# Kernel tuning notes

Hardware: AMD Instinct MI355X
Metric: run time of the kernel (lower is better)

The kernel has to match this reference:

```python
import jax, jax.numpy as jnp
import numpy as np

N, E, B = 50000, 400000, 50
F_IN, HID, HEADS, F_OUT = 128, 32, 8, 64
HC = HID * HEADS  # 256


def gat_conv(x, src, dst, W, a_s, a_d, b, n):
    """PyG-style GATConv (concat=True, negative_slope=0.2), inference mode."""
    H, C = a_s.shape
    h = (x @ W).reshape(n, H, C)                       # [N,H,C]
    alpha_s = (h * a_s).sum(-1)                        # [N,H]
    alpha_d = (h * a_d).sum(-1)                        # [N,H]
    logits = jax.nn.leaky_relu(alpha_s[src] + alpha_d[dst], 0.2)  # [E,H]
    m = jax.ops.segment_max(logits, dst, num_segments=n)
    m = jnp.where(jnp.isfinite(m), m, 0.0)
    e = jnp.exp(logits - m[dst])
    den = jax.ops.segment_sum(e, dst, num_segments=n)
    alpha = e / (den[dst] + 1e-16)                     # segment softmax over dst
    out = jax.ops.segment_sum(h[src] * alpha[:, :, None], dst, num_segments=n)
    return out.reshape(n, H * C) + b


def setup_inputs() -> dict:
    key = jax.random.key(0)
    ks = jax.random.split(key, 24)
    s = 0.1
    inp = {
        "x": jax.random.normal(ks[0], (N, F_IN), jnp.float32),
        "edge_index": jax.random.randint(ks[1], (2, E), 0, N),
        "batch": jnp.sort(jax.random.randint(ks[2], (N,), 0, B)),
        "W1": jax.random.normal(ks[3], (F_IN, HC), jnp.float32) * s,
        "a_src1": jax.random.normal(ks[4], (HEADS, HID), jnp.float32) * s,
        "a_dst1": jax.random.normal(ks[5], (HEADS, HID), jnp.float32) * s,
        "b1": jnp.zeros((HC,), jnp.float32),
        "W2": jax.random.normal(ks[6], (HC, HC), jnp.float32) * s,
        "a_src2": jax.random.normal(ks[7], (1, HC), jnp.float32) * s,
        "a_dst2": jax.random.normal(ks[8], (1, HC), jnp.float32) * s,
        "b2": jnp.zeros((HC,), jnp.float32),
        "W3": jax.random.normal(ks[9], (HC, HC), jnp.float32) * s,
        "a_src3": jax.random.normal(ks[10], (1, HC), jnp.float32) * s,
        "a_dst3": jax.random.normal(ks[11], (1, HC), jnp.float32) * s,
        "b3": jnp.zeros((HC,), jnp.float32),
        "W4": jax.random.normal(ks[12], (HC, F_OUT), jnp.float32) * s,
        "a_src4": jax.random.normal(ks[13], (1, F_OUT), jnp.float32) * s,
        "a_dst4": jax.random.normal(ks[14], (1, F_OUT), jnp.float32) * s,
        "b4": jnp.zeros((F_OUT,), jnp.float32),
        "Wl": jax.random.normal(ks[15], (F_OUT, 1), jnp.float32) * s,
        "bl": jnp.zeros((1,), jnp.float32),
    }
    return inp


def reference(x, edge_index, batch, W1, a_src1, a_dst1, b1, W2, a_src2, a_dst2, b2,
              W3, a_src3, a_dst3, b3, W4, a_src4, a_dst4, b4, Wl, bl):
    n = x.shape[0]
    loop = jnp.arange(n)
    src = jnp.concatenate([edge_index[0], loop])  # add self loops (PyG default)
    dst = jnp.concatenate([edge_index[1], loop])
    x = jax.nn.elu(gat_conv(x, src, dst, W1, a_src1, a_dst1, b1, n))
    x = jax.nn.elu(gat_conv(x, src, dst, W2, a_src2, a_dst2, b2, n))
    x = jax.nn.elu(gat_conv(x, src, dst, W3, a_src3, a_dst3, b3, n))
    x_gat = gat_conv(x, src, dst, W4, a_src4, a_dst4, b4, n)
    # to_dense_batch(x_gat, batch).mean(dim=1): sum per graph / max graph size
    counts = jax.ops.segment_sum(jnp.ones((n,), x_gat.dtype), batch, num_segments=B)
    max_nodes = counts.max()
    pooled = jax.ops.segment_sum(x_gat, batch, num_segments=B) / max_nodes  # [B,F_OUT]
    return pooled @ Wl + bl  # [B,1]
```

## Files before the change

### kernel.cpp

```cpp
#include <hip/hip_runtime.h>
#include <math.h>


typedef __attribute__((ext_vector_type(8))) short short8;
typedef __attribute__((ext_vector_type(4))) float f32x4;

__device__ __forceinline__ unsigned short f2bf(float f) {
  unsigned int u = __builtin_bit_cast(unsigned int, f);
  unsigned int r = u + 0x7FFFu + ((u >> 16) & 1u);
  return (unsigned short)(r >> 16);
}
__device__ __forceinline__ float bf2f(unsigned short h) {
  unsigned int u = ((unsigned int)h) << 16;
  return __builtin_bit_cast(float, u);
}
__device__ __forceinline__ unsigned short f2h(float f) {
  _Float16 h = (_Float16)f;
  return __builtin_bit_cast(unsigned short, h);
}
__device__ __forceinline__ float h2f(unsigned short u) {
  return (float)__builtin_bit_cast(_Float16, u);
}

__device__ __forceinline__ void fma_mix_lo(float& acc, unsigned int packed, float w) {
  asm("v_fma_mix_f32 %0, %1, %2, %0 op_sel_hi:[1,0,0]"
      : "+v"(acc) : "v"(packed), "v"(w));
}
__device__ __forceinline__ void fma_mix_hi(float& acc, unsigned int packed, float w) {
  asm("v_fma_mix_f32 %0, %1, %2, %0 op_sel:[1,0,0] op_sel_hi:[1,0,0]"
      : "+v"(acc) : "v"(packed), "v"(w));
}

__device__ __forceinline__ void gload16(const unsigned short* g, unsigned short* l) {
  __builtin_amdgcn_global_load_lds(
      (const __attribute__((address_space(1))) void*)g,
      (__attribute__((address_space(3))) void*)l, 16, 0, 0);
}

template<int H>
__global__ __launch_bounds__(256) void k_gemm_mfma(
    const unsigned short* __restrict__ A2, const unsigned short* __restrict__ Wt,
    unsigned short* __restrict__ C, const float* __restrict__ avec_s,
    const float* __restrict__ avec_d, float* __restrict__ outS,
    float* __restrict__ outD, int M, int Kb, int Nc)
{
  __shared__ unsigned short lds[12288];
  unsigned short* As = lds;
  unsigned short* Bs = lds + 4096;
  const int tid = threadIdx.x;
  const int w = tid >> 6, l = tid & 63;
  const int row0 = blockIdx.x * 64, col0 = blockIdx.y * 128;
  const int wr = w >> 1, wc = w & 1;
  const int fr = l & 15, kg = l >> 4;
  const int xr = (fr & 7) << 4;
  const int sK = Kb;
  const int csrc = 8 * ((l & 7) ^ ((l >> 3) & 7));
  const int lrow = l >> 3;

  f32x4 acc[2][4];
  #pragma unroll
  for (int i = 0; i < 2; i++)
    #pragma unroll
    for (int j = 0; j < 4; j++) acc[i][j] = (f32x4){0.f, 0.f, 0.f, 0.f};

  for (int kp = 0; kp < sK; kp += 64) {
    #pragma unroll
    for (int i = 0; i < 2; i++) {
      int q = w * 2 + i;
      gload16(&A2[(size_t)(row0 + q * 8 + lrow) * sK + (kp + csrc)], &As[q * 512]);
    }
    #pragma unroll
    for (int i = 0; i < 4; i++) {
      int q = w * 4 + i;
      gload16(&Wt[(size_t)(col0 + q * 8 + lrow) * sK + (kp + csrc)], &Bs[q * 512]);
    }
    __syncthreads();
    #pragma unroll
    for (int kk = 0; kk < 2; kk++) {
      short8 a[2], b[4];
      #pragma unroll
      for (int mi = 0; mi < 2; mi++) {
        int r = wr * 32 + mi * 16 + fr;
        int off = r * 128 + ((kk * 64 + kg * 16) ^ xr);
        a[mi] = *(const short8*)((const char*)As + off);
      }
      #pragma unroll
      for (int ni = 0; ni < 4; ni++) {
        int c = wc * 64 + ni * 16 + fr;
        int off = c * 128 + ((kk * 64 + kg * 16) ^ xr);
        b[ni] = *(const short8*)((const char*)Bs + off);
      }
      #pragma unroll
      for (int mi = 0; mi < 2; mi++)
        #pragma unroll
        for (int ni = 0; ni < 4; ni++)
          acc[mi][ni] = __builtin_amdgcn_mfma_f32_16x16x32_bf16(
              a[mi], b[ni], acc[mi][ni], 0, 0, 0);
    }
    __syncthreads();
  }

  #pragma unroll
  for (int mi = 0; mi < 2; mi++)
    #pragma unroll
    for (int ni = 0; ni < 4; ni++)
      #pragma unroll
      for (int rr = 0; rr < 4; rr++) {
        int row = wr * 32 + mi * 16 + kg * 4 + rr;
        int c = wc * 64 + ni * 16 + fr;
        int sc = c ^ (((row >> 1) & 7) << 3);
        lds[row * 128 + sc] = f2h(acc[mi][ni][rr]);
      }
  __syncthreads();

  constexpr int RW = (H == 8) ? 4 : 16;
  const int Ch = Nc / H;
  const int rbase = tid >> 4;
  const int cc = tid & 15;
  const int c0 = cc * 8;
  const int gc0 = col0 + c0;
  float as8[8], ad8[8];
  #pragma unroll
  for (int j = 0; j < 8; j++) {
    bool ok = (gc0 + j) < Nc;
    as8[j] = ok ? avec_s[gc0 + j] : 0.f;
    ad8[j] = ok ? avec_d[gc0 + j] : 0.f;
  }
  #pragma unroll
  for (int i = 0; i < 4; i++) {
    int row = rbase + i * 16;
    int gr = row0 + row;
    int scc = c0 ^ (((row >> 1) & 7) << 3);
    short8 cv = *(const short8*)&lds[row * 128 + scc];
    if (gr < M && gc0 < Nc)
      *(short8*)&C[(size_t)gr * Nc + gc0] = cv;
    float ps = 0.f, pd = 0.f;
    #pragma unroll
    for (int j = 0; j < 8; j++) {
      float cf = h2f((unsigned short)cv[j]);
      ps = fmaf(cf, as8[j], ps);
      pd = fmaf(cf, ad8[j], pd);
    }
    #pragma unroll
    for (int off = 1; off < RW; off <<= 1) {
      ps += __shfl_xor(ps, off);
      pd += __shfl_xor(pd, off);
    }
    if ((tid & (RW - 1)) == 0 && gr < M) {
      int head = gc0 / Ch;
      atomicAdd(&outS[gr * H + head], ps);
      atomicAdd(&outD[gr * H + head], pd);
    }
  }
}

__global__ __launch_bounds__(256) void k_packX(const float* __restrict__ x,
    unsigned short* __restrict__ A2, int N, int Mpad)
{
  int row = blockIdx.x * 8 + (threadIdx.x >> 5);
  int c = (threadIdx.x & 31) * 4;
  if (row >= Mpad) return;
  float4 v = make_float4(0.f, 0.f, 0.f, 0.f);
  if (row < N) v = *(const float4*)&x[(size_t)row * 128 + c];
  unsigned short h0 = f2bf(v.x), h1 = f2bf(v.y), h2 = f2bf(v.z), h3 = f2bf(v.w);
  *(uint2*)&A2[(size_t)row * 128 + c] =
      make_uint2((unsigned)h0 | ((unsigned)h1 << 16),
                 (unsigned)h2 | ((unsigned)h3 << 16));
}

__device__ __forceinline__ void packW_one(const float* __restrict__ W,
    unsigned short* __restrict__ Wt, int K, int NC, int idx)
{
  int c = idx / K, k = idx % K;
  unsigned short o = 0;
  if (c < NC) o = f2bf(W[(size_t)k * NC + c]);
  Wt[(size_t)c * K + k] = o;
}

__global__ void k_packW_all(const float* __restrict__ W1, const float* __restrict__ W2,
    const float* __restrict__ W3, const float* __restrict__ W4,
    unsigned short* __restrict__ t1, unsigned short* __restrict__ t2,
    unsigned short* __restrict__ t3, unsigned short* __restrict__ t4)
{
  int idx = blockIdx.x * 256 + threadIdx.x;
  if (idx < 32768)            packW_one(W1, t1, 128, 256, idx);
  else if (idx < 98304)       packW_one(W2, t2, 256, 256, idx - 32768);
  else if (idx < 163840)      packW_one(W3, t3, 256, 256, idx - 98304);
  else if (idx < 196608)      packW_one(W4, t4, 256,  64, idx - 163840);
}

template<int H>
__global__ void k_wcomp(const float* __restrict__ aS, const float* __restrict__ aD,
    const int* __restrict__ col, const int* __restrict__ rid,
    float* __restrict__ wbuf, int M)
{
  int idx = blockIdx.x * 256 + threadIdx.x;
  if (idx >= M) return;
  int e = idx / H, hd = idx % H;
  int s = col[e], r = rid[e];
  float lg = aS[s * H + hd] + aD[r * H + hd];
  lg = fmaxf(lg, 0.2f * lg);
  wbuf[idx] = __expf(lg);
}

template<int H, int HC, int ELU, int SPLIT>
__global__ __launch_bounds__(256) void k_aggregate(const unsigned short* __restrict__ h,
    const float* __restrict__ wbuf,
    const int* __restrict__ rowptr, const int* __restrict__ col,
    const float* __restrict__ bias, float* __restrict__ xout,
    unsigned short* __restrict__ a2out, int N)
{
  constexpr int VEC = HC / 64;
  constexpr int C = HC / H;
  constexpr int CH = (H == 8) ? 8 : 64;
  __shared__ float wlds[4][64];
  int wave = threadIdx.x >> 6, lane = threadIdx.x & 63;
  int row = blockIdx.x * 4 + wave;
  if (row >= N) return;
  const int cb = lane * VEC;
  const int hdg = cb / C;
  int s0 = rowptr[row], s1 = rowptr[row + 1];

  float den = 0.f;
  float acc[VEC];
  #pragma unroll
  for (int v = 0; v < VEC; v++) acc[v] = 0.f;

  for (int base = s0; base < s1; base += CH) {
    int cnt = min(CH, s1 - base);
    int eo = (H == 8) ? (lane >> 3) : lane;
    bool valid = eo < cnt;
    int s = col[valid ? (base + eo) : (s1 - 1)];
    float wv = valid ? wbuf[(unsigned)(base * H) + lane] : 0.f;
    float d = wv;
    if constexpr (H == 8) {
      d += __shfl_xor(d, 8); d += __shfl_xor(d, 16); d += __shfl_xor(d, 32);
      wlds[wave][lane] = wv;
    } else {
      #pragma unroll
      for (int off = 1; off < 64; off <<= 1) d += __shfl_xor(d, off);
    }
    den += d;
    if (H == 8) {
      asm volatile("s_waitcnt lgkmcnt(0)" ::: "memory");
    }
    #pragma unroll 4
    for (int j = 0; j < cnt; j++) {
      int sj = __builtin_amdgcn_readlane(s, (H == 8) ? (j * 8) : j);
      float wj;
      if constexpr (H == 8) {
        wj = wlds[wave][j * 8 + hdg];
      } else {
        wj = __builtin_bit_cast(float,
              __builtin_amdgcn_readlane(__builtin_bit_cast(int, wv), j));
      }
      unsigned off = (unsigned)sj * HC + cb;
      if constexpr (VEC == 4) {
        uint2 raw = *(const uint2*)(h + off);
        fma_mix_lo(acc[0], raw.x, wj);
        fma_mix_hi(acc[1], raw.x, wj);
        fma_mix_lo(acc[2], raw.y, wj);
        fma_mix_hi(acc[3], raw.y, wj);
      } else {
        unsigned int raw = h[off];
        fma_mix_lo(acc[0], raw, wj);
      }
    }
  }
  if (H == 8) den = __shfl(den, hdg);
  float inv = 1.f / (den + 1e-16f);
  float o[VEC];
  #pragma unroll
  for (int v = 0; v < VEC; v++) {
    float t = acc[v] * inv + bias[cb + v];
    if (ELU) t = t > 0.f ? t : expm1f(t);
    o[v] = t;
  }
  if constexpr (SPLIT) {
    unsigned short hi[4];
    #pragma unroll
    for (int v = 0; v < 4; v++) hi[v] = f2bf(o[v]);
    *(uint2*)&a2out[(size_t)row * HC + cb] =
        make_uint2((unsigned)hi[0] | ((unsigned)hi[1] << 16),
                   (unsigned)hi[2] | ((unsigned)hi[3] << 16));
  } else if constexpr (VEC == 4) {
    *(float4*)&xout[(size_t)row * HC + cb] = make_float4(o[0], o[1], o[2], o[3]);
  } else {
    xout[(size_t)row * HC + cb] = o[0];
  }
}

__global__ void k_init(int* deg, float* pool, unsigned short* A2, int N, int B,
                       int Mpad) {
  int i = blockIdx.x * 256 + threadIdx.x;
  if (i < N) deg[i] = 1;
  if (i < B * 64) pool[i] = 0.f;
  int padn = (Mpad - N) * 256;
  if (i < padn) A2[(size_t)N * 256 + i] = 0;
}

__global__ void k_deg(const int* __restrict__ ei, int* deg, int E) {
  int e = blockIdx.x * 256 + threadIdx.x;
  if (e < E) atomicAdd(&deg[ei[E + e]], 1);
}

__global__ __launch_bounds__(256) void k_scan1(const int* __restrict__ deg,
                                               int* csum, int N, int chunk) {
  int bid = blockIdx.x, t = threadIdx.x;
  int lo = bid * chunk, hi = min(lo + chunk, N);
  int s = 0;
  for (int i = lo + t; i < hi; i += 256) s += deg[i];
  #pragma unroll
  for (int off = 32; off; off >>= 1) s += __shfl_xor(s, off);
  __shared__ int sh[4];
  if ((t & 63) == 0) sh[t >> 6] = s;
  __syncthreads();
  if (t == 0) csum[bid] = sh[0] + sh[1] + sh[2] + sh[3];
}

__global__ __launch_bounds__(256) void k_scan2(const int* __restrict__ csum,
    int* coff, const int* __restrict__ bat, int* cnt, int N, int B) {
  __shared__ int s[256];
  int t = threadIdx.x;
  int v0 = csum[t];
  s[t] = v0;
  for (int off = 1; off < 256; off <<= 1) {
    __syncthreads();
    int v = (t >= off) ? s[t - off] : 0;
    __syncthreads();
    s[t] += v;
  }
  __syncthreads();
  coff[t] = s[t] - v0;
  if (t < B) {
    int lo0 = 0, hi0 = N;
    while (lo0 < hi0) { int mid = (lo0 + hi0) >> 1; if (bat[mid] < t) lo0 = mid + 1; else hi0 = mid; }
    int lo1 = lo0, hi1 = N;
    while (lo1 < hi1) { int mid = (lo1 + hi1) >> 1; if (bat[mid] < t + 1) lo1 = mid + 1; else hi1 = mid; }
    cnt[t] = lo1 - lo0;
  }
}

__global__ __launch_bounds__(256) void k_scan3(const int* __restrict__ deg,
    const int* __restrict__ coff, int* rowptr, int* cursor, int N, int chunk) {
  __shared__ int s[256];
  int bid = blockIdx.x, t = threadIdx.x;
  int i = bid * chunk + t;
  int v = (t < chunk && i < N) ? deg[i] : 0;
  s[t] = v;
  for (int off = 1; off < 256; off <<= 1) {
    __syncthreads();
    int x = (t >= off) ? s[t - off] : 0;
    __syncthreads();
    s[t] += x;
  }
  __syncthreads();
  int excl = s[t] - v + coff[bid];
  if (t < chunk && i < N) {
    rowptr[i] = excl;
    cursor[i] = excl;
    if (i == N - 1) rowptr[N] = excl + v;
  }
}

__global__ void k_scatter(const int* __restrict__ ei, int* cursor, int* col,
                          int* rid, int E, int N) {
  int idx = blockIdx.x * 256 + threadIdx.x;
  if (idx >= E + N) return;
  int s, d;
  if (idx < E) { s = ei[idx]; d = ei[E + idx]; }
  else         { s = d = idx - E; }
  int pos = atomicAdd(&cursor[d], 1);
  col[pos] = s;
  rid[pos] = d;
}

__global__ __launch_bounds__(256) void k_pool(const float* __restrict__ xg,
    const int* __restrict__ bat, float* pool, int N) {
  int lane = threadIdx.x & 63, w = threadIdx.x >> 6;
  int base = (blockIdx.x * 4 + w) * 16;
  if (base >= N) return;
  int end = min(base + 16, N);
  float local = 0.f;
  int curb = bat[base];
  for (int n = base; n < end; n++) {
    int b = bat[n];
    if (b != curb) {
      atomicAdd(&pool[curb * 64 + lane], local);
      local = 0.f; curb = b;
    }
    local += xg[(size_t)n * 64 + lane];
  }
  atomicAdd(&pool[curb * 64 + lane], local);
}

__global__ void k_final(const float* __restrict__ pool, const int* __restrict__ cnt,
    const float* __restrict__ Wl, const float* __restrict__ bl,
    float* __restrict__ out, int B) {
  int lane = threadIdx.x;
  int c = (lane < B) ? cnt[lane] : 0;
  #pragma unroll
  for (int off = 32; off; off >>= 1) c = max(c, __shfl_xor(c, off));
  float invm = 1.f / (float)c;
  float wl = Wl[lane];
  for (int b = 0; b < B; b++) {
    float ps = pool[b * 64 + lane] * wl;
    #pragma unroll
    for (int off = 32; off; off >>= 1) ps += __shfl_xor(ps, off);
    if (lane == 0) out[b] = ps * invm + bl[0];
  }
}

extern "C" void kernel_launch(void* const* d_in, const int* in_sizes, int n_in,
                              void* d_out, int out_size, void* d_ws, size_t ws_size,
                              hipStream_t stream)
{
  (void)n_in; (void)ws_size;
  const float* x   = (const float*)d_in[0];
  const int*   ei  = (const int*)d_in[1];
  const int*   bat = (const int*)d_in[2];
  const float* W1  = (const float*)d_in[3];
  const float* as1 = (const float*)d_in[4];
  const float* ad1 = (const float*)d_in[5];
  const float* b1  = (const float*)d_in[6];
  const float* W2  = (const float*)d_in[7];
  const float* as2 = (const float*)d_in[8];
  const float* ad2 = (const float*)d_in[9];
  const float* b2  = (const float*)d_in[10];
  const float* W3  = (const float*)d_in[11];
  const float* as3 = (const float*)d_in[12];
  const float* ad3 = (const float*)d_in[13];
  const float* b3  = (const float*)d_in[14];
  const float* W4  = (const float*)d_in[15];
  const float* as4 = (const float*)d_in[16];
  const float* ad4 = (const float*)d_in[17];
  const float* b4  = (const float*)d_in[18];
  const float* Wl  = (const float*)d_in[19];
  const float* bl  = (const float*)d_in[20];
  float* out = (float*)d_out;

  const int N = in_sizes[0] / 128;
  const int E = in_sizes[1] / 2;
  const int B = out_size;
  const int Mpad = ((N + 127) / 128) * 128;
  const int EN = E + N;

  char* p = (char*)d_ws;
  auto alloc = [&](size_t bytes) -> void* {
    void* r = (void*)p;
    p += ((bytes + 255) & ~(size_t)255);
    return r;
  };
  unsigned short* A2 = (unsigned short*)alloc((size_t)Mpad * 256 * 2);
  unsigned short* hbuf = (unsigned short*)alloc((size_t)N * 256 * 2);
  unsigned short* w2t1 = (unsigned short*)alloc((size_t)256 * 128 * 2);
  unsigned short* w2t2 = (unsigned short*)alloc((size_t)256 * 256 * 2);
  unsigned short* w2t3 = (unsigned short*)alloc((size_t)256 * 256 * 2);
  unsigned short* w2t4 = (unsigned short*)alloc((size_t)128 * 256 * 2);
  float* aAll  = (float*)alloc((size_t)N * 22 * 4);
  float* aSb   = aAll;
  float* aDb   = aAll + (size_t)N * 11;
  float* wbuf  = (float*)alloc((size_t)EN * 8 * 4);
  int*   deg   = (int*)alloc((size_t)N * 4);
  int*   rowptr= (int*)alloc((size_t)(N + 1) * 4);
  int*   cursor= (int*)alloc((size_t)N * 4);
  int*   col   = (int*)alloc((size_t)EN * 4);
  int*   rid   = (int*)alloc((size_t)EN * 4);
  int*   csum  = (int*)alloc(256 * 4);
  int*   coff  = (int*)alloc(256 * 4);
  float* pool  = (float*)alloc((size_t)B * 64 * 4);
  int*   cnt   = (int*)alloc((size_t)B * 4);
  float* xpool = (float*)A2;

  const int chunk = (N + 255) / 256;
  dim3 T(256);

  k_init<<<dim3((N + 255) / 256), T, 0, stream>>>(deg, pool, A2, N, B, Mpad);
  k_deg<<<dim3((E + 255) / 256), T, 0, stream>>>(ei, deg, E);
  k_scan1<<<dim3(256), T, 0, stream>>>(deg, csum, N, chunk);
  k_scan2<<<dim3(1), T, 0, stream>>>(csum, coff, bat, cnt, N, B);
  k_scan3<<<dim3(256), T, 0, stream>>>(deg, coff, rowptr, cursor, N, chunk);
  k_scatter<<<dim3((EN + 255) / 256), T, 0, stream>>>(ei, cursor, col, rid, E, N);
  hipMemsetAsync(aAll, 0, (size_t)N * 22 * 4, stream);

  k_packX<<<dim3(Mpad / 8), T, 0, stream>>>(x, A2, N, Mpad);
  k_packW_all<<<dim3(768), T, 0, stream>>>(W1, W2, W3, W4, w2t1, w2t2, w2t3, w2t4);

  dim3 nwav((N + 3) / 4);
  dim3 g2(Mpad / 64, 2), g1(Mpad / 64, 1);
  dim3 gw8((EN * 8 + 255) / 256), gw1((EN + 255) / 256);

  float* aS1 = aSb;                 float* aD1 = aDb;
  float* aS2 = aSb + (size_t)N * 8; float* aD2 = aDb + (size_t)N * 8;
  float* aS3 = aSb + (size_t)N * 9; float* aD3 = aDb + (size_t)N * 9;
  float* aS4 = aSb + (size_t)N * 10;float* aD4 = aDb + (size_t)N * 10;

  k_gemm_mfma<8><<<g2, T, 0, stream>>>(A2, w2t1, hbuf, as1, ad1, aS1, aD1, N, 128, 256);
  k_wcomp<8><<<gw8, T, 0, stream>>>(aS1, aD1, col, rid, wbuf, EN * 8);
  k_aggregate<8, 256, 1, 1><<<nwav, T, 0, stream>>>(hbuf, wbuf, rowptr, col, b1,
                                                    nullptr, A2, N);
  k_gemm_mfma<1><<<g2, T, 0, stream>>>(A2, w2t2, hbuf, as2, ad2, aS2, aD2, N, 256, 256);
  k_wcomp<1><<<gw1, T, 0, stream>>>(aS2, aD2, col, rid, wbuf, EN);
  k_aggregate<1, 256, 1, 1><<<nwav, T, 0, stream>>>(hbuf, wbuf, rowptr, col, b2,
                                                    nullptr, A2, N);
  k_gemm_mfma<1><<<g2, T, 0, stream>>>(A2, w2t3, hbuf, as3, ad3, aS3, aD3, N, 256, 256);
  k_wcomp<1><<<gw1, T, 0, stream>>>(aS3, aD3, col, rid, wbuf, EN);
  k_aggregate<1, 256, 1, 1><<<nwav, T, 0, stream>>>(hbuf, wbuf, rowptr, col, b3,
                                                    nullptr, A2, N);
  k_gemm_mfma<1><<<g1, T, 0, stream>>>(A2, w2t4, hbuf, as4, ad4, aS4, aD4, N, 256, 64);
  k_wcomp<1><<<gw1, T, 0, stream>>>(aS4, aD4, col, rid, wbuf, EN);
  k_aggregate<1, 64, 0, 0><<<nwav, T, 0, stream>>>(hbuf, wbuf, rowptr, col, b4,
                                                   xpool, nullptr, N);

  k_pool<<<dim3((N + 63) / 64), T, 0, stream>>>(xpool, bat, pool, N);
  k_final<<<dim3(1), dim3(64), 0, stream>>>(pool, cnt, Wl, bl, out, B);
}
```

Before: 419.2 us.

## Use one-wave blocks for aggregation and split HC=64 layer across edge groups

Aggregation kernels now launch one 64-thread block per destination row instead of four rows per 256-thread block, which reduces tail imbalance from rows with uneven degree. The final 64-channel layer is restructured so that four 16-lane groups each process a different edge in parallel, using 4-wide loads, with a cross-group shuffle reduction at the end. Before, that layer used one scalar load per lane. The x packing kernel is also merged into the weight packing kernel to save one launch. The risk is more blocks to schedule and more LDS round trips.

```diff
diff --git a/kernel.cpp b/kernel.cpp
--- a/kernel.cpp
+++ b/kernel.cpp
@@ -154,20 +154,6 @@
   }
 }
 
-__global__ __launch_bounds__(256) void k_packX(const float* __restrict__ x,
-    unsigned short* __restrict__ A2, int N, int Mpad)
-{
-  int row = blockIdx.x * 8 + (threadIdx.x >> 5);
-  int c = (threadIdx.x & 31) * 4;
-  if (row >= Mpad) return;
-  float4 v = make_float4(0.f, 0.f, 0.f, 0.f);
-  if (row < N) v = *(const float4*)&x[(size_t)row * 128 + c];
-  unsigned short h0 = f2bf(v.x), h1 = f2bf(v.y), h2 = f2bf(v.z), h3 = f2bf(v.w);
-  *(uint2*)&A2[(size_t)row * 128 + c] =
-      make_uint2((unsigned)h0 | ((unsigned)h1 << 16),
-                 (unsigned)h2 | ((unsigned)h3 << 16));
-}
-
 __device__ __forceinline__ void packW_one(const float* __restrict__ W,
     unsigned short* __restrict__ Wt, int K, int NC, int idx)
 {
@@ -177,16 +163,30 @@
   Wt[(size_t)c * K + k] = o;
 }
 
-__global__ void k_packW_all(const float* __restrict__ W1, const float* __restrict__ W2,
+__global__ void k_pack_all(const float* __restrict__ W1, const float* __restrict__ W2,
     const float* __restrict__ W3, const float* __restrict__ W4,
     unsigned short* __restrict__ t1, unsigned short* __restrict__ t2,
-    unsigned short* __restrict__ t3, unsigned short* __restrict__ t4)
+    unsigned short* __restrict__ t3, unsigned short* __restrict__ t4,
+    const float* __restrict__ x, unsigned short* __restrict__ A2,
+    int N, int Mpad)
 {
   int idx = blockIdx.x * 256 + threadIdx.x;
   if (idx < 32768)            packW_one(W1, t1, 128, 256, idx);
   else if (idx < 98304)       packW_one(W2, t2, 256, 256, idx - 32768);
   else if (idx < 163840)      packW_one(W3, t3, 256, 256, idx - 98304);
   else if (idx < 196608)      packW_one(W4, t4, 256,  64, idx - 163840);
+  else {
+    int t = idx - 196608;
+    int row = t >> 5;
+    if (row >= Mpad) return;
+    int c = (t & 31) * 4;
+    float4 v = make_float4(0.f, 0.f, 0.f, 0.f);
+    if (row < N) v = *(const float4*)&x[(size_t)row * 128 + c];
+    unsigned short h0 = f2bf(v.x), h1 = f2bf(v.y), h2 = f2bf(v.z), h3 = f2bf(v.w);
+    *(uint2*)&A2[(size_t)row * 128 + c] =
+        make_uint2((unsigned)h0 | ((unsigned)h1 << 16),
+                   (unsigned)h2 | ((unsigned)h3 << 16));
+  }
 }
 
 template<int H>
@@ -204,89 +204,128 @@
 }
 
 template<int H, int HC, int ELU, int SPLIT>
-__global__ __launch_bounds__(256) void k_aggregate(const unsigned short* __restrict__ h,
+__global__ __launch_bounds__(64) void k_aggregate(const unsigned short* __restrict__ h,
     const float* __restrict__ wbuf,
     const int* __restrict__ rowptr, const int* __restrict__ col,
     const float* __restrict__ bias, float* __restrict__ xout,
     unsigned short* __restrict__ a2out, int N)
 {
-  constexpr int VEC = HC / 64;
-  constexpr int C = HC / H;
-  constexpr int CH = (H == 8) ? 8 : 64;
-  __shared__ float wlds[4][64];
-  int wave = threadIdx.x >> 6, lane = threadIdx.x & 63;
-  int row = blockIdx.x * 4 + wave;
+  const int lane = threadIdx.x;
+  const int row = blockIdx.x;
   if (row >= N) return;
-  const int cb = lane * VEC;
-  const int hdg = cb / C;
   int s0 = rowptr[row], s1 = rowptr[row + 1];
-
   float den = 0.f;
-  float acc[VEC];
-  #pragma unroll
-  for (int v = 0; v < VEC; v++) acc[v] = 0.f;
-
-  for (int base = s0; base < s1; base += CH) {
-    int cnt = min(CH, s1 - base);
-    int eo = (H == 8) ? (lane >> 3) : lane;
-    bool valid = eo < cnt;
-    int s = col[valid ? (base + eo) : (s1 - 1)];
-    float wv = valid ? wbuf[(unsigned)(base * H) + lane] : 0.f;
-    float d = wv;
-    if constexpr (H == 8) {
-      d += __shfl_xor(d, 8); d += __shfl_xor(d, 16); d += __shfl_xor(d, 32);
-      wlds[wave][lane] = wv;
-    } else {
-      #pragma unroll
-      for (int off = 1; off < 64; off <<= 1) d += __shfl_xor(d, off);
-    }
-    den += d;
-    if (H == 8) {
-      asm volatile("s_waitcnt lgkmcnt(0)" ::: "memory");
-    }
-    #pragma unroll 4
-    for (int j = 0; j < cnt; j++) {
-      int sj = __builtin_amdgcn_readlane(s, (H == 8) ? (j * 8) : j);
-      float wj;
+
+  if constexpr (HC == 256) {
+    constexpr int C = HC / H;
+    constexpr int CH = (H == 8) ? 8 : 64;
+    __shared__ float wlds[(H == 8) ? 64 : 1];
+    const int cb = lane * 4;
+    const int hdg = cb / C;
+    float acc[4] = {0.f, 0.f, 0.f, 0.f};
+    for (int base = s0; base < s1; base += CH) {
+      int cnt = min(CH, s1 - base);
+      int eo = (H == 8) ? (lane >> 3) : lane;
+      bool valid = eo < cnt;
+      int s = col[valid ? (base + eo) : (s1 - 1)];
+      float wv = valid ? wbuf[(unsigned)(base * H) + lane] : 0.f;
+      float d = wv;
       if constexpr (H == 8) {
-        wj = wlds[wave][j * 8 + hdg];
+        d += __shfl_xor(d, 8); d += __shfl_xor(d, 16); d += __shfl_xor(d, 32);
+        wlds[lane] = wv;
       } else {
-        wj = __builtin_bit_cast(float,
-              __builtin_amdgcn_readlane(__builtin_bit_cast(int, wv), j));
-      }
-      unsigned off = (unsigned)sj * HC + cb;
-      if constexpr (VEC == 4) {
+        #pragma unroll
+        for (int off = 1; off < 64; off <<= 1) d += __shfl_xor(d, off);
+      }
+      den += d;
+      if (H == 8) {
+        asm volatile("s_waitcnt lgkmcnt(0)" ::: "memory");
+      }
+      #pragma unroll 4
+      for (int j = 0; j < cnt; j++) {
+        int sj = __builtin_amdgcn_readlane(s, (H == 8) ? (j * 8) : j);
+        float wj;
+        if constexpr (H == 8) {
+          wj = wlds[j * 8 + hdg];
+        } else {
+          wj = __builtin_bit_cast(float,
+                __builtin_amdgcn_readlane(__builtin_bit_cast(int, wv), j));
+        }
+        unsigned off = (unsigned)sj * HC + cb;
         uint2 raw = *(const uint2*)(h + off);
         fma_mix_lo(acc[0], raw.x, wj);
         fma_mix_hi(acc[1], raw.x, wj);
         fma_mix_lo(acc[2], raw.y, wj);
         fma_mix_hi(acc[3], raw.y, wj);
-      } else {
-        unsigned int raw = h[off];
-        fma_mix_lo(acc[0], raw, wj);
-      }
-    }
-  }
-  if (H == 8) den = __shfl(den, hdg);
-  float inv = 1.f / (den + 1e-16f);
-  float o[VEC];
-  #pragma unroll
-  for (int v = 0; v < VEC; v++) {
-    float t = acc[v] * inv + bias[cb + v];
-    if (ELU) t = t > 0.f ? t : expm1f(t);
-    o[v] = t;
-  }
-  if constexpr (SPLIT) {
-    unsigned short hi[4];
-    #pragma unroll
-    for (int v = 0; v < 4; v++) hi[v] = f2bf(o[v]);
-    *(uint2*)&a2out[(size_t)row * HC + cb] =
-        make_uint2((unsigned)hi[0] | ((unsigned)hi[1] << 16),
-                   (unsigned)hi[2] | ((unsigned)hi[3] << 16));
-  } else if constexpr (VEC == 4) {
-    *(float4*)&xout[(size_t)row * HC + cb] = make_float4(o[0], o[1], o[2], o[3]);
+      }
+    }
+    if (H == 8) den = __shfl(den, hdg);
+    float inv = 1.f / (den + 1e-16f);
+    float o[4];
+    #pragma unroll
+    for (int v = 0; v < 4; v++) {
+      float t = acc[v] * inv + bias[cb + v];
+      if (ELU) t = t > 0.f ? t : expm1f(t);
+      o[v] = t;
+    }
+    if constexpr (SPLIT) {
+      unsigned short hi[4];
+      #pragma unroll
+      for (int v = 0; v < 4; v++) hi[v] = f2bf(o[v]);
+      *(uint2*)&a2out[(size_t)row * HC + cb] =
+          make_uint2((unsigned)hi[0] | ((unsigned)hi[1] << 16),
+                     (unsigned)hi[2] | ((unsigned)hi[3] << 16));
+    } else {
+      *(float4*)&xout[(size_t)row * HC + cb] = make_float4(o[0], o[1], o[2], o[3]);
+    }
   } else {
-    xout[(size_t)row * HC + cb] = o[0];
+    __shared__ float wlds[64];
+    __shared__ int   slds[64];
+    const int cb = (lane & 15) * 4;
+    const int g = lane >> 4;
+    float acc[4] = {0.f, 0.f, 0.f, 0.f};
+    for (int base = s0; base < s1; base += 64) {
+      int cnt = min(64, s1 - base);
+      bool valid = lane < cnt;
+      int s = col[valid ? (base + lane) : (s1 - 1)];
+      float wv = valid ? wbuf[(unsigned)base + lane] : 0.f;
+      float d = wv;
+      #pragma unroll
+      for (int off = 1; off < 64; off <<= 1) d += __shfl_xor(d, off);
+      den += d;
+      wlds[lane] = wv;
+      slds[lane] = s;
+      asm volatile("s_waitcnt lgkmcnt(0)" ::: "memory");
+      __builtin_amdgcn_sched_barrier(0);
+      #pragma unroll 2
+      for (int j = 0; j < cnt; j += 4) {
+        int e = j + g;
+        float wj = wlds[e];
+        int sj = slds[e];
+        unsigned off = (unsigned)sj * 64 + cb;
+        uint2 raw = *(const uint2*)(h + off);
+        fma_mix_lo(acc[0], raw.x, wj);
+        fma_mix_hi(acc[1], raw.x, wj);
+        fma_mix_lo(acc[2], raw.y, wj);
+        fma_mix_hi(acc[3], raw.y, wj);
+      }
+    }
+    #pragma unroll
+    for (int v = 0; v < 4; v++) {
+      acc[v] += __shfl_xor(acc[v], 16);
+      acc[v] += __shfl_xor(acc[v], 32);
+    }
+    if (g == 0) {
+      float inv = 1.f / (den + 1e-16f);
+      float o[4];
+      #pragma unroll
+      for (int v = 0; v < 4; v++) {
+        float t = acc[v] * inv + bias[cb + v];
+        if (ELU) t = t > 0.f ? t : expm1f(t);
+        o[v] = t;
+      }
+      *(float4*)&xout[(size_t)row * 64 + cb] = make_float4(o[0], o[1], o[2], o[3]);
+    }
   }
 }
 
@@ -474,6 +513,7 @@
 
   const int chunk = (N + 255) / 256;
   dim3 T(256);
+  dim3 T64(64);
 
   k_init<<<dim3((N + 255) / 256), T, 0, stream>>>(deg, pool, A2, N, B, Mpad);
   k_deg<<<dim3((E + 255) / 256), T, 0, stream>>>(ei, deg, E);
@@ -483,10 +523,10 @@
   k_scatter<<<dim3((EN + 255) / 256), T, 0, stream>>>(ei, cursor, col, rid, E, N);
   hipMemsetAsync(aAll, 0, (size_t)N * 22 * 4, stream);
 
-  k_packX<<<dim3(Mpad / 8), T, 0, stream>>>(x, A2, N, Mpad);
-  k_packW_all<<<dim3(768), T, 0, stream>>>(W1, W2, W3, W4, w2t1, w2t2, w2t3, w2t4);
-
-  dim3 nwav((N + 3) / 4);
+  k_pack_all<<<dim3((196608 + Mpad * 32 + 255) / 256), T, 0, stream>>>(
+      W1, W2, W3, W4, w2t1, w2t2, w2t3, w2t4, x, A2, N, Mpad);
+
+  dim3 nrow(N);
   dim3 g2(Mpad / 64, 2), g1(Mpad / 64, 1);
   dim3 gw8((EN * 8 + 255) / 256), gw1((EN + 255) / 256);
 
@@ -497,21 +537,21 @@
 
   k_gemm_mfma<8><<<g2, T, 0, stream>>>(A2, w2t1, hbuf, as1, ad1, aS1, aD1, N, 128, 256);
   k_wcomp<8><<<gw8, T, 0, stream>>>(aS1, aD1, col, rid, wbuf, EN * 8);
-  k_aggregate<8, 256, 1, 1><<<nwav, T, 0, stream>>>(hbuf, wbuf, rowptr, col, b1,
-                                                    nullptr, A2, N);
+  k_aggregate<8, 256, 1, 1><<<nrow, T64, 0, stream>>>(hbuf, wbuf, rowptr, col, b1,
+                                                      nullptr, A2, N);
   k_gemm_mfma<1><<<g2, T, 0, stream>>>(A2, w2t2, hbuf, as2, ad2, aS2, aD2, N, 256, 256);
   k_wcomp<1><<<gw1, T, 0, stream>>>(aS2, aD2, col, rid, wbuf, EN);
-  k_aggregate<1, 256, 1, 1><<<nwav, T, 0, stream>>>(hbuf, wbuf, rowptr, col, b2,
-                                                    nullptr, A2, N);
+  k_aggregate<1, 256, 1, 1><<<nrow, T64, 0, stream>>>(hbuf, wbuf, rowptr, col, b2,
+                                                      nullptr, A2, N);
   k_gemm_mfma<1><<<g2, T, 0, stream>>>(A2, w2t3, hbuf, as3, ad3, aS3, aD3, N, 256, 256);
   k_wcomp<1><<<gw1, T, 0, stream>>>(aS3, aD3, col, rid, wbuf, EN);
-  k_aggregate<1, 256, 1, 1><<<nwav, T, 0, stream>>>(hbuf, wbuf, rowptr, col, b3,
-                                                    nullptr, A2, N);
+  k_aggregate<1, 256, 1, 1><<<nrow, T64, 0, stream>>>(hbuf, wbuf, rowptr, col, b3,
+                                                      nullptr, A2, N);
   k_gemm_mfma<1><<<g1, T, 0, stream>>>(A2, w2t4, hbuf, as4, ad4, aS4, aD4, N, 256, 64);
   k_wcomp<1><<<gw1, T, 0, stream>>>(aS4, aD4, col, rid, wbuf, EN);
-  k_aggregate<1, 64, 0, 0><<<nwav, T, 0, stream>>>(hbuf, wbuf, rowptr, col, b4,
-                                                   xpool, nullptr, N);
+  k_aggregate<1, 64, 0, 0><<<nrow, T64, 0, stream>>>(hbuf, wbuf, rowptr, col, b4,
+                                                     xpool, nullptr, N);
 
   k_pool<<<dim3((N + 63) / 64), T, 0, stream>>>(xpool, bat, pool, N);
-  k_final<<<dim3(1), dim3(64), 0, stream>>>(pool, cnt, Wl, bl, out, B);
-}
+  k_final<<<dim3(1), T64, 0, stream>>>(pool, cnt, Wl, bl, out, B);
+}
```

Result: faster. 386.8 us (-7.7%).
